# Optimization experiments

Measured on AMD Instinct MI355X. Metric: run time of the kernel, lower is better.

Reference implementation:

```python
import jax, jax.numpy as jnp
import numpy as np


def setup_inputs() -> dict:
    key = jax.random.key(0)
    k1, k2 = jax.random.split(key)
    B, S, H = 32, 4096, 1024
    output = jax.random.normal(k1, (B, 1, H), dtype=jnp.float32)
    context = jax.random.normal(k2, (B, S, H), dtype=jnp.float32)
    return {"output": output, "context": context}


def reference(output, context):
    # scores: (B, 1, S) = q @ k^T
    attn = jnp.einsum('bqh,bsh->bqs', output, context)
    attn = jax.nn.softmax(attn, axis=2)
    # out: (B, 1, H) = attn @ context, then tanh
    out = jnp.tanh(jnp.einsum('bqs,bsh->bqh', attn, context))
    return (out, attn)
```

## Files before the change

### kernel.cpp

```cpp
#include <hip/hip_runtime.h>
#include <math.h>

constexpr int kB  = 32;
constexpr int kS  = 4096;
constexpr int kH  = 1024;
constexpr int kNC = 64;
constexpr int kCH = kS / kNC;
constexpr int WPB = 4;
constexpr int NP  = kCH / 2;

#define GLOAD_LDS16(gp, lp)                                                        \
  __builtin_amdgcn_global_load_lds(                                               \
      (const __attribute__((address_space(1))) void*)(gp),                        \
      (__attribute__((address_space(3))) void*)(lp), 16, 0, 0)

__device__ __forceinline__ void stage_row(const float* __restrict__ g,
                                          float* l, int lane) {
  #pragma unroll
  for (int j = 0; j < 4; ++j)
    GLOAD_LDS16(g + j * 256 + 4 * lane, l + j * 256);
}

#define PAIR4(acc4, w04, w14) \
  acc4.x = fmaf(p1, w14.x, fmaf(p0, w04.x, acc4.x * sc)); \
  acc4.y = fmaf(p1, w14.y, fmaf(p0, w04.y, acc4.y * sc)); \
  acc4.z = fmaf(p1, w14.z, fmaf(p0, w04.z, acc4.z * sc)); \
  acc4.w = fmaf(p1, w14.w, fmaf(p0, w04.w, acc4.w * sc));

__global__ __launch_bounds__(256, 2) void attn_pass1(
    const float* __restrict__ q,
    const float* __restrict__ ctx,
    float* __restrict__ scores,
    float* __restrict__ pm,
    float* __restrict__ pl,
    float* __restrict__ pacc)
{
  __shared__ __align__(16) float lds[WPB * 2 * 2048];

  const int lane = threadIdx.x & 63;
  const int wid  = threadIdx.x >> 6;
  const int wave = blockIdx.x * WPB + wid;
  const int b    = wave / kNC;
  const int c    = wave % kNC;

  float* wbuf = &lds[wid * 4096];

  const float4* qp = reinterpret_cast<const float4*>(q + (size_t)b * kH) + lane;
  const float4 Qa = qp[0], Qb = qp[64], Qc = qp[128], Qd = qp[192];

  const float* cbase = ctx + ((size_t)b * kS + (size_t)c * kCH) * kH;

  float m = -3.0e38f, l = 0.0f;
  float4 aa = make_float4(0.f,0.f,0.f,0.f), ab = aa, ac = aa, ad = aa;
  float myscore = 0.0f;

  auto compute_pair = [&](int t) {
    const float4* p0 = reinterpret_cast<const float4*>(wbuf + (t & 1) * 2048) + lane;
    const float4* p1 = p0 + 256;

    const float4 w0a = p0[0], w0b = p0[64], w0c = p0[128], w0d = p0[192];
    const float4 w1a = p1[0], w1b = p1[64], w1c = p1[128], w1d = p1[192];

    float d0, d1;
    d0  = w0a.x*Qa.x + w0a.y*Qa.y + w0a.z*Qa.z + w0a.w*Qa.w;
    d0 += w0b.x*Qb.x + w0b.y*Qb.y + w0b.z*Qb.z + w0b.w*Qb.w;
    d0 += w0c.x*Qc.x + w0c.y*Qc.y + w0c.z*Qc.z + w0c.w*Qc.w;
    d0 += w0d.x*Qd.x + w0d.y*Qd.y + w0d.z*Qd.z + w0d.w*Qd.w;
    d1  = w1a.x*Qa.x + w1a.y*Qa.y + w1a.z*Qa.z + w1a.w*Qa.w;
    d1 += w1b.x*Qb.x + w1b.y*Qb.y + w1b.z*Qb.z + w1b.w*Qb.w;
    d1 += w1c.x*Qc.x + w1c.y*Qc.y + w1c.z*Qc.z + w1c.w*Qc.w;
    d1 += w1d.x*Qd.x + w1d.y*Qd.y + w1d.z*Qd.z + w1d.w*Qd.w;

    #pragma unroll
    for (int off = 32; off >= 1; off >>= 1) {
      d0 += __shfl_xor(d0, off, 64);
      d1 += __shfl_xor(d1, off, 64);
    }

    if (lane == 2 * t)     myscore = d0;
    if (lane == 2 * t + 1) myscore = d1;

    const float nm = fmaxf(m, fmaxf(d0, d1));
    const float sc = __expf(m - nm);
    const float p0s = __expf(d0 - nm);
    const float p1s = __expf(d1 - nm);
    m = nm;
    l = fmaf(l, sc, p0s + p1s);
    { const float p0 = p0s, p1 = p1s;
      PAIR4(aa, w0a, w1a); PAIR4(ab, w0b, w1b);
      PAIR4(ac, w0c, w1c); PAIR4(ad, w0d, w1d); }
  };

  stage_row(cbase,        wbuf,        lane);
  stage_row(cbase + 1024, wbuf + 1024, lane);

  for (int t = 0; t < NP - 1; ++t) {
    const float* g  = cbase + (size_t)(t + 1) * 2048;
    float*       lb = wbuf + ((t + 1) & 1) * 2048;
    stage_row(g,        lb,        lane);
    stage_row(g + 1024, lb + 1024, lane);
    asm volatile("s_waitcnt vmcnt(8)" ::: "memory");
    compute_pair(t);
  }
  asm volatile("s_waitcnt vmcnt(0)" ::: "memory");
  compute_pair(NP - 1);

  scores[(size_t)b * kS + (size_t)c * kCH + lane] = myscore;
  if (lane == 0) { pm[wave] = m; pl[wave] = l; }
  float4* pap = reinterpret_cast<float4*>(pacc + (size_t)wave * kH) + lane;
  pap[0] = aa; pap[64] = ab; pap[128] = ac; pap[192] = ad;
}

__global__ __launch_bounds__(256) void attn_combine(
    const float* __restrict__ scores,
    const float* __restrict__ pm,
    const float* __restrict__ pl,
    const float* __restrict__ pacc,
    float* __restrict__ out)
{
  const int b  = blockIdx.x;
  const int by = blockIdx.y;
  const int t  = threadIdx.x;

  __shared__ float red[256];
  __shared__ float wgt[kNC];

  const float mi = (t < kNC) ? pm[b * kNC + t] : -3.0e38f;
  red[t] = mi;
  __syncthreads();
  #pragma unroll
  for (int o = 128; o >= 1; o >>= 1) {
    if (t < o) red[t] = fmaxf(red[t], red[t + o]);
    __syncthreads();
  }
  const float m_g = red[0];
  __syncthreads();

  float li = 0.0f, wi = 0.0f;
  if (t < kNC) {
    wi = __expf(mi - m_g);
    li = pl[b * kNC + t] * wi;
  }
  red[t] = li;
  __syncthreads();
  #pragma unroll
  for (int o = 128; o >= 1; o >>= 1) {
    if (t < o) red[t] += red[t + o];
    __syncthreads();
  }
  const float inv = 1.0f / red[0];
  if (t < kNC) wgt[t] = wi * inv;
  __syncthreads();

  if (by < 8) {
    __shared__ float4 sh4[8][32];
    const int h4     = t & 31;
    const int stripe = t >> 5;
    const float4* base =
        reinterpret_cast<const float4*>(pacc + ((size_t)(b * kNC + stripe)) * kH + by * 128) + h4;
    const size_t istep = (size_t)8 * (kH / 4);

    float4 s = make_float4(0.f, 0.f, 0.f, 0.f);
    #pragma unroll 8
    for (int k = 0; k < kNC / 8; ++k) {
      const float w = wgt[stripe + 8 * k];
      const float4 v = base[(size_t)k * istep];
      s.x = fmaf(w, v.x, s.x); s.y = fmaf(w, v.y, s.y);
      s.z = fmaf(w, v.z, s.z); s.w = fmaf(w, v.w, s.w);
    }
    sh4[stripe][h4] = s;
    __syncthreads();

    if (t < 32) {
      float4 r = sh4[0][t];
      #pragma unroll
      for (int i = 1; i < 8; ++i) {
        const float4 v = sh4[i][t];
        r.x += v.x; r.y += v.y; r.z += v.z; r.w += v.w;
      }
      r.x = tanhf(r.x); r.y = tanhf(r.y);
      r.z = tanhf(r.z); r.w = tanhf(r.w);
      reinterpret_cast<float4*>(out + (size_t)b * kH + by * 128)[t] = r;
    }
  } else {
    const float4* sb = reinterpret_cast<const float4*>(scores + (size_t)b * kS);
    float4* abuf = reinterpret_cast<float4*>(out + (size_t)kB * kH + (size_t)b * kS);
    #pragma unroll
    for (int k = 0; k < kS / 4 / 256; ++k) {
      const int i = k * 256 + t;
      float4 v = sb[i];
      v.x = __expf(v.x - m_g) * inv; v.y = __expf(v.y - m_g) * inv;
      v.z = __expf(v.z - m_g) * inv; v.w = __expf(v.w - m_g) * inv;
      abuf[i] = v;
    }
  }
}

extern "C" void kernel_launch(void* const* d_in, const int* in_sizes, int n_in,
                              void* d_out, int out_size, void* d_ws, size_t ws_size,
                              hipStream_t stream) {
  const float* q   = (const float*)d_in[0];
  const float* ctx = (const float*)d_in[1];
  float* out = (float*)d_out;
  float* ws  = (float*)d_ws;

  float* scores = ws;
  float* pm     = scores + (size_t)kB * kS;
  float* pl     = pm + kB * kNC;
  float* pacc   = pl + kB * kNC;

  attn_pass1<<<dim3(kB * kNC / WPB), 256, 0, stream>>>(q, ctx, scores, pm, pl, pacc);
  attn_combine<<<dim3(kB, 9), 256, 0, stream>>>(scores, pm, pl, pacc, out);
}
```

Measured before the change: 110.5 us.

## Deepen pass1 LDS prefetch ring to five row slots and shrink blocks

Pass1 now stages context rows through a 5-slot per-wave LDS ring instead of a 2-pair double buffer. It keeps roughly four rows in flight and issues the next row's load after computing each pair, so more global memory latency is hidden. Blocks shrink to 2 waves (128 threads), which changes per-CU occupancy and LDS use per block. The combine kernel replaces its LDS tree reductions and many __syncthreads with wave shuffle reductions over the 64 chunk stats. The ring indexing with modulo adds a little address arithmetic, and the vmcnt counts must match exactly.

```diff
diff --git a/kernel.cpp b/kernel.cpp
--- a/kernel.cpp
+++ b/kernel.cpp
@@ -6,8 +6,9 @@
 constexpr int kH  = 1024;
 constexpr int kNC = 64;
 constexpr int kCH = kS / kNC;
-constexpr int WPB = 4;
+constexpr int WPB = 2;
 constexpr int NP  = kCH / 2;
+constexpr int NSLOT = 5;
 
 #define GLOAD_LDS16(gp, lp)                                                        \
   __builtin_amdgcn_global_load_lds(                                               \
@@ -27,7 +28,7 @@
   acc4.z = fmaf(p1, w14.z, fmaf(p0, w04.z, acc4.z * sc)); \
   acc4.w = fmaf(p1, w14.w, fmaf(p0, w04.w, acc4.w * sc));
 
-__global__ __launch_bounds__(256, 2) void attn_pass1(
+__global__ __launch_bounds__(128, 2) void attn_pass1(
     const float* __restrict__ q,
     const float* __restrict__ ctx,
     float* __restrict__ scores,
@@ -35,7 +36,7 @@
     float* __restrict__ pl,
     float* __restrict__ pacc)
 {
-  __shared__ __align__(16) float lds[WPB * 2 * 2048];
+  __shared__ __align__(16) float lds[WPB * NSLOT * 1024];
 
   const int lane = threadIdx.x & 63;
   const int wid  = threadIdx.x >> 6;
@@ -43,7 +44,7 @@
   const int b    = wave / kNC;
   const int c    = wave % kNC;
 
-  float* wbuf = &lds[wid * 4096];
+  float* wbuf = &lds[wid * NSLOT * 1024];
 
   const float4* qp = reinterpret_cast<const float4*>(q + (size_t)b * kH) + lane;
   const float4 Qa = qp[0], Qb = qp[64], Qc = qp[128], Qd = qp[192];
@@ -54,9 +55,9 @@
   float4 aa = make_float4(0.f,0.f,0.f,0.f), ab = aa, ac = aa, ad = aa;
   float myscore = 0.0f;
 
-  auto compute_pair = [&](int t) {
-    const float4* p0 = reinterpret_cast<const float4*>(wbuf + (t & 1) * 2048) + lane;
-    const float4* p1 = p0 + 256;
+  auto compute_pair = [&](int t, const float* buf0, const float* buf1) {
+    const float4* p0 = reinterpret_cast<const float4*>(buf0) + lane;
+    const float4* p1 = reinterpret_cast<const float4*>(buf1) + lane;
 
     const float4 w0a = p0[0], w0b = p0[64], w0c = p0[128], w0d = p0[192];
     const float4 w1a = p1[0], w1b = p1[64], w1c = p1[128], w1d = p1[192];
@@ -91,19 +92,27 @@
       PAIR4(ac, w0c, w1c); PAIR4(ad, w0d, w1d); }
   };
 
-  stage_row(cbase,        wbuf,        lane);
-  stage_row(cbase + 1024, wbuf + 1024, lane);
-
-  for (int t = 0; t < NP - 1; ++t) {
-    const float* g  = cbase + (size_t)(t + 1) * 2048;
-    float*       lb = wbuf + ((t + 1) & 1) * 2048;
-    stage_row(g,        lb,        lane);
-    stage_row(g + 1024, lb + 1024, lane);
-    asm volatile("s_waitcnt vmcnt(8)" ::: "memory");
-    compute_pair(t);
+  stage_row(cbase + 0 * 1024, wbuf + 0 * 1024, lane);
+  stage_row(cbase + 1 * 1024, wbuf + 1 * 1024, lane);
+  stage_row(cbase + 2 * 1024, wbuf + 2 * 1024, lane);
+  stage_row(cbase + 3 * 1024, wbuf + 3 * 1024, lane);
+
+  for (int t = 0; t < NP - 2; ++t) {
+    const int r0 = 2 * t + 4;
+    stage_row(cbase + (size_t)r0 * 1024, wbuf + (r0 % NSLOT) * 1024, lane);
+    asm volatile("s_waitcnt vmcnt(12)" ::: "memory");
+    compute_pair(t, wbuf + ((2 * t) % NSLOT) * 1024,
+                    wbuf + ((2 * t + 1) % NSLOT) * 1024);
+    asm volatile("" ::: "memory");
+    const int r1 = 2 * t + 5;
+    stage_row(cbase + (size_t)r1 * 1024, wbuf + (r1 % NSLOT) * 1024, lane);
   }
+  asm volatile("s_waitcnt vmcnt(8)" ::: "memory");
+  compute_pair(NP - 2, wbuf + ((2 * (NP - 2)) % NSLOT) * 1024,
+                       wbuf + ((2 * (NP - 2) + 1) % NSLOT) * 1024);
   asm volatile("s_waitcnt vmcnt(0)" ::: "memory");
-  compute_pair(NP - 1);
+  compute_pair(NP - 1, wbuf + ((2 * (NP - 1)) % NSLOT) * 1024,
+                       wbuf + ((2 * (NP - 1) + 1) % NSLOT) * 1024);
 
   scores[(size_t)b * kS + (size_t)c * kCH + lane] = myscore;
   if (lane == 0) { pm[wave] = m; pl[wave] = l; }
@@ -122,34 +131,22 @@
   const int by = blockIdx.y;
   const int t  = threadIdx.x;
 
-  __shared__ float red[256];
   __shared__ float wgt[kNC];
-
-  const float mi = (t < kNC) ? pm[b * kNC + t] : -3.0e38f;
-  red[t] = mi;
-  __syncthreads();
-  #pragma unroll
-  for (int o = 128; o >= 1; o >>= 1) {
-    if (t < o) red[t] = fmaxf(red[t], red[t + o]);
-    __syncthreads();
+  __shared__ float2 stat_sh;
+
+  if (t < 64) {
+    const float mi = pm[b * kNC + t];
+    float mg = mi;
+    #pragma unroll
+    for (int off = 32; off >= 1; off >>= 1) mg = fmaxf(mg, __shfl_xor(mg, off, 64));
+    const float wi = __expf(mi - mg);
+    float li = pl[b * kNC + t] * wi;
+    #pragma unroll
+    for (int off = 32; off >= 1; off >>= 1) li += __shfl_xor(li, off, 64);
+    const float inv = 1.0f / li;
+    wgt[t] = wi * inv;
+    if (t == 0) stat_sh = make_float2(mg, inv);
   }
-  const float m_g = red[0];
-  __syncthreads();
-
-  float li = 0.0f, wi = 0.0f;
-  if (t < kNC) {
-    wi = __expf(mi - m_g);
-    li = pl[b * kNC + t] * wi;
-  }
-  red[t] = li;
-  __syncthreads();
-  #pragma unroll
-  for (int o = 128; o >= 1; o >>= 1) {
-    if (t < o) red[t] += red[t + o];
-    __syncthreads();
-  }
-  const float inv = 1.0f / red[0];
-  if (t < kNC) wgt[t] = wi * inv;
   __syncthreads();
 
   if (by < 8) {
@@ -183,6 +180,7 @@
       reinterpret_cast<float4*>(out + (size_t)b * kH + by * 128)[t] = r;
     }
   } else {
+    const float m_g = stat_sh.x, inv = stat_sh.y;
     const float4* sb = reinterpret_cast<const float4*>(scores + (size_t)b * kS);
     float4* abuf = reinterpret_cast<float4*>(out + (size_t)kB * kH + (size_t)b * kS);
     #pragma unroll
@@ -209,6 +207,6 @@
   float* pl     = pm + kB * kNC;
   float* pacc   = pl + kB * kNC;
 
-  attn_pass1<<<dim3(kB * kNC / WPB), 256, 0, stream>>>(q, ctx, scores, pm, pl, pacc);
+  attn_pass1<<<dim3(kB * kNC / WPB), 128, 0, stream>>>(q, ctx, scores, pm, pl, pacc);
   attn_combine<<<dim3(kB, 9), 256, 0, stream>>>(scores, pm, pl, pacc, out);
 }
```

Result: faster. 104.9 us (-5.0%).
